# Kernel optimization log

Hardware: AMD Instinct MI355X
Metric: run time of the kernel (lower is better)

## Reference

```python
import jax, jax.numpy as jnp
import numpy as np

DIM = 512   # model dim C (num_heads=1 -> head_dim = C)
NK = 128    # tokens per key-batch element
BQ = 512    # query batch
BK = 256    # key batch
NC = 1000   # num_classes for visual_fc head


def _ln(x, g, b, eps=1e-5):
    m = x.mean(-1, keepdims=True)
    v = x.var(-1, keepdims=True)
    return (x - m) * jax.lax.rsqrt(v + eps) * g + b


def _l2norm(x, eps=1e-12):  # F.normalize(p=2, dim=-1)
    n = jnp.linalg.norm(x, axis=-1, keepdims=True)
    return x / jnp.maximum(n, eps)


def setup_inputs() -> dict:
    key = jax.random.key(0)
    ks = jax.random.split(key, 8)
    s = 0.02
    return {
        "qx": jax.random.normal(ks[0], (BQ, 1, DIM), dtype=jnp.float32),
        "kx": jax.random.normal(ks[1], (BK, NK, DIM), dtype=jnp.float32),
        "key_padding_mask": jax.random.randint(ks[2], (BK, NK), 0, 2).astype(bool),
        "logit_scale": jnp.array([np.log(100.0)], dtype=jnp.float32),
        "g_q": jnp.ones((DIM,), jnp.float32), "b_q": jnp.zeros((DIM,), jnp.float32),
        "g_k": jnp.ones((DIM,), jnp.float32), "b_k": jnp.zeros((DIM,), jnp.float32),
        "wq": jax.random.normal(ks[3], (DIM, DIM), dtype=jnp.float32) * s,
        "wk": jax.random.normal(ks[4], (DIM, DIM), dtype=jnp.float32) * s,
        "w1": jax.random.normal(ks[5], (4 * DIM, DIM), dtype=jnp.float32) * s,
        "b1": jnp.zeros((4 * DIM,), jnp.float32),
        "w2": jax.random.normal(ks[6], (NC, 4 * DIM), dtype=jnp.float32) * s,
        "b2": jnp.zeros((NC,), jnp.float32),
    }


def reference(qx, kx, key_padding_mask, logit_scale,
              g_q, b_q, g_k, b_k, wq, wk, w1, b1, w2, b2):
    C = qx.shape[-1]
    scale = C ** -0.5  # num_heads=1 so head_dim == C
    # cross-batch single-query attention (Attention.forward)
    q = _ln(qx, g_q, b_q) @ wq.T                       # [Bq,1,C]
    k = _ln(kx, g_k, b_k) @ wk.T                       # [Bk,Nk,C]
    attn = jnp.einsum('qoc,knc->qkn', q, k) * scale    # [Bq,Bk,Nk]
    attn = jnp.where(key_padding_mask[None, :, :], -jnp.inf, attn)
    attn = jax.nn.softmax(attn, axis=-1)
    v = jnp.einsum('knc,qkn->qkc', kx, attn)           # [Bq,Bk,C]
    # two_branch head
    h = jax.nn.relu(qx[:, 0, :] @ w1.T + b1)           # [Bq,4C]
    x1 = h @ w2.T + b2                                 # [Bq,NC]
    x2 = jnp.einsum('qkc,qoc->qk', _l2norm(v), _l2norm(qx)) * jnp.exp(logit_scale)[0]
    return (x1, x2)
```

## Files before the change

### kernel.cpp

```cpp
#include <hip/hip_runtime.h>

typedef unsigned short u16;
typedef unsigned int u32;
typedef short bf16x8s __attribute__((ext_vector_type(8)));
typedef float f32x4 __attribute__((ext_vector_type(4)));

#define SCALE_C 0.044194173824159216f
#define MFMA16 __builtin_amdgcn_mfma_f32_16x16x32_bf16

__device__ __forceinline__ u16 f2bf(float f){
  union { float f; u32 u; } c; c.f = f;
  u32 u = c.u;
  return (u16)((u + 0x7fffu + ((u >> 16) & 1u)) >> 16);
}

__device__ __forceinline__ void gload16(const void* g, void* l){
  __builtin_amdgcn_global_load_lds((const __attribute__((address_space(1))) void*)g,
                                   (__attribute__((address_space(3))) void*)l, 16, 0, 0);
}

#define OFF_KXB  ((size_t)0)
#define OFF_G    (OFF_KXB + 33554432)
#define OFF_W2B  (OFF_G + 8388608)
#define OFF_H    (OFF_W2B + 4096000)
#define OFF_W1B  (OFF_H + 2097152)
#define OFF_QLN  (OFF_W1B + 2097152)
#define OFF_QHAT (OFF_QLN + 524288)
#define OFF_QXB  (OFF_QHAT + 524288)
#define OFF_P    (OFF_QXB + 524288)
#define OFF_M2   (OFF_P + 524288)
#define OFF_WQB  (OFF_M2 + 524288)
#define OFF_WCT  (OFF_WQB + 524288)
#define OFF_KM   (OFF_WCT + 524288)
#define OFF_KR   (OFF_KM + 131072)
#define OFF_T2   (OFF_KR + 131072)
#define OFF_FLAG (OFF_T2 + 4096)

__global__ __launch_bounds__(512) void k_phase1(
    const float* __restrict__ qx, const float* __restrict__ kx,
    const int* __restrict__ maskw,
    const float* __restrict__ g_q, const float* __restrict__ b_q,
    const float* __restrict__ wq, const float* __restrict__ wk,
    const float* __restrict__ w1, const float* __restrict__ w2,
    const float* __restrict__ b2,
    u16* __restrict__ kxb, float* __restrict__ km, float* __restrict__ kr,
    u16* __restrict__ Gm,
    u16* __restrict__ qln, u16* __restrict__ qhat, u16* __restrict__ qxb,
    u16* __restrict__ wct, u16* __restrict__ w1b, u16* __restrict__ w2b,
    float* __restrict__ t2s, int* __restrict__ flag, float* __restrict__ x1o)
{
  __shared__ __align__(16) u16 lBig[16384];
  __shared__ float redq[8][2];
  __shared__ int smax;
  const int bid = blockIdx.x, tid = threadIdx.x;
  const int lane = tid & 63, w = tid >> 6;
  const int l15 = lane & 15, lg = lane >> 4;

  if (bid < 256){
    u16* lk = lBig;
    const int z = bid;
    const int a0 = (w>>2)*64, b0 = (w&3)*32;
    float s[16] = {0,0,0,0,0,0,0,0,0,0,0,0,0,0,0,0};
    float sq[16] = {0,0,0,0,0,0,0,0,0,0,0,0,0,0,0,0};
    f32x4 acc[4][2] = {};
    for (int ch = 0; ch < 4; ch++){
      #pragma unroll
      for (int i = 0; i < 16; i++){
        int r = w*16 + i;
        float2 v = *(const float2*)(kx + ((size_t)z*128 + r)*512 + ch*128 + lane*2);
        s[i] += v.x + v.y; sq[i] += v.x*v.x + v.y*v.y;
        u32 pk = f2bf(v.x) | ((u32)f2bf(v.y)<<16);
        *(u32*)(kxb + ((size_t)z*128 + r)*512 + ch*128 + lane*2) = pk;
        *(u32*)&lk[r*128 + ((lane*2) ^ ((r&7)<<3))] = pk;
      }
      __syncthreads();
      #pragma unroll
      for (int kk = 0; kk < 4; kk++){
        int cgr = kk*4 + lg;
        bf16x8s a[4], b[2];
        #pragma unroll
        for (int i2 = 0; i2 < 4; i2++){
          int r = a0 + i2*16 + l15;
          a[i2] = *(const bf16x8s*)&lk[r*128 + ((cgr*8) ^ ((r&7)<<3))];
        }
        #pragma unroll
        for (int j = 0; j < 2; j++){
          int r = b0 + j*16 + l15;
          b[j] = *(const bf16x8s*)&lk[r*128 + ((cgr*8) ^ ((r&7)<<3))];
        }
        #pragma unroll
        for (int i2 = 0; i2 < 4; i2++)
          #pragma unroll
          for (int j = 0; j < 2; j++)
            acc[i2][j] = MFMA16(a[i2], b[j], acc[i2][j], 0,0,0);
      }
      __syncthreads();
    }
    #pragma unroll
    for (int i = 0; i < 16; i++){
      float ss = s[i], qq = sq[i];
      #pragma unroll
      for (int o = 1; o < 64; o <<= 1){ ss += __shfl_xor(ss,o); qq += __shfl_xor(qq,o); }
      if (lane == 0){
        int r = w*16 + i;
        float mean = ss*(1.0f/512.0f);
        float var  = qq*(1.0f/512.0f) - mean*mean;
        km[z*128+r] = mean; kr[z*128+r] = rsqrtf(var + 1e-5f);
      }
    }
    u16* G = Gm + (size_t)z*16384;
    #pragma unroll
    for (int i2 = 0; i2 < 4; i2++)
      #pragma unroll
      for (int j = 0; j < 2; j++)
        #pragma unroll
        for (int r = 0; r < 4; r++)
          G[(size_t)(a0 + i2*16 + lg*4 + r)*128 + b0 + j*16 + l15] = f2bf(acc[i2][j][r]);
  } else if (bid < 512){
    const int row = (bid-256)*2 + (tid>>8);
    const int t = tid & 255;
    float2 v = *(const float2*)(qx + (size_t)row*512 + t*2);
    float s = v.x+v.y, sq = v.x*v.x+v.y*v.y;
    #pragma unroll
    for (int o = 1; o < 64; o <<= 1){ s += __shfl_xor(s,o); sq += __shfl_xor(sq,o); }
    if (lane == 0){ redq[w][0]=s; redq[w][1]=sq; }
    __syncthreads();
    const int h4 = (tid>>8)*4;
    s  = redq[h4][0]+redq[h4+1][0]+redq[h4+2][0]+redq[h4+3][0];
    sq = redq[h4][1]+redq[h4+1][1]+redq[h4+2][1]+redq[h4+3][1];
    float mean = s*(1.0f/512.0f);
    float var  = sq*(1.0f/512.0f) - mean*mean;
    float rstd = rsqrtf(var + 1e-5f);
    float il2  = 1.0f / fmaxf(sqrtf(sq), 1e-12f);
    float2 g  = *(const float2*)(g_q + t*2);
    float2 bb = *(const float2*)(b_q + t*2);
    u32 a  = f2bf((v.x-mean)*rstd*g.x+bb.x) | ((u32)f2bf((v.y-mean)*rstd*g.y+bb.y)<<16);
    u32 hh = f2bf(v.x*il2) | ((u32)f2bf(v.y*il2)<<16);
    u32 xx = f2bf(v.x)     | ((u32)f2bf(v.y)<<16);
    *(u32*)(qln  + (size_t)row*512 + t*2) = a;
    *(u32*)(qhat + (size_t)row*512 + t*2) = hh;
    *(u32*)(qxb  + (size_t)row*512 + t*2) = xx;
  } else if (bid < 2024){
    const float* in; u16* out; int i;
    if (bid < 1024) { in = w1; out = w1b; i = (bid-512)*512 + tid; }
    else            { in = w2; out = w2b; i = (bid-1024)*512 + tid; }
    float4 v = *(const float4*)(in + (size_t)i*4);
    uint2 p;
    p.x = f2bf(v.x)|((u32)f2bf(v.y)<<16); p.y = f2bf(v.z)|((u32)f2bf(v.w)<<16);
    *(uint2*)(out + (size_t)i*4) = p;
  } else if (bid < 2088){
    const int t = bid - 2024;
    const int f0 = (t>>3)*64, c0 = (t&7)*64;
    const int w4 = w & 3;
    const int wr = (w4>>1)*32, wc = (w4&1)*32;
    u16* shA = lBig;
    u16* shB = lBig + 4096;
    f32x4 acc[2][2] = {};
    for (int i0 = 0; i0 < 512; i0 += 64){
      const int ii = tid >> 3;
      const int cc8 = (tid & 7) * 8;
      float4 va0 = *(const float4*)(wk + (size_t)(i0+ii)*512 + f0 + cc8);
      float4 va1 = *(const float4*)(wk + (size_t)(i0+ii)*512 + f0 + cc8 + 4);
      float4 vb0 = *(const float4*)(wq + (size_t)(i0+ii)*512 + c0 + cc8);
      float4 vb1 = *(const float4*)(wq + (size_t)(i0+ii)*512 + c0 + cc8 + 4);
      #pragma unroll
      for (int e = 0; e < 8; e++){
        float fa = e < 4 ? (&va0.x)[e] : (&va1.x)[e-4];
        float fb = e < 4 ? (&vb0.x)[e] : (&vb1.x)[e-4];
        int rowc = cc8 + e;
        int idx = rowc*64 + (((ii>>3) ^ (rowc&7))*8 + (ii&7));
        shA[idx] = f2bf(fa);
        shB[idx] = f2bf(fb);
      }
      __syncthreads();
      #pragma unroll
      for (int kk = 0; kk < 2; kk++){
        int cgr = kk*4 + lg;
        int ra0 = wr + l15, ra1 = wr + 16 + l15;
        int rb0 = wc + l15, rb1 = wc + 16 + l15;
        bf16x8s a0 = *(const bf16x8s*)&shA[ra0*64 + ((cgr ^ (ra0&7))*8)];
        bf16x8s a1 = *(const bf16x8s*)&shA[ra1*64 + ((cgr ^ (ra1&7))*8)];
        bf16x8s b0 = *(const bf16x8s*)&shB[rb0*64 + ((cgr ^ (rb0&7))*8)];
        bf16x8s b1 = *(const bf16x8s*)&shB[rb1*64 + ((cgr ^ (rb1&7))*8)];
        acc[0][0]=MFMA16(a0,b0,acc[0][0],0,0,0);
        acc[0][1]=MFMA16(a0,b1,acc[0][1],0,0,0);
        acc[1][0]=MFMA16(a1,b0,acc[1][0],0,0,0);
        acc[1][1]=MFMA16(a1,b1,acc[1][1],0,0,0);
      }
      __syncthreads();
    }
    if (tid < 256){
      #pragma unroll
      for (int i = 0; i < 2; i++)
        #pragma unroll
        for (int j = 0; j < 2; j++)
          #pragma unroll
          for (int r = 0; r < 4; r++)
            wct[(size_t)(f0 + wr + i*16 + lg*4 + r)*512 + c0 + wc + j*16 + l15]
                = f2bf(acc[i][j][r]);
    }
  } else if (bid < 2338){
    int i = (bid-2088)*2048 + tid*4;
    #pragma unroll
    for (int e = 0; e < 4; e++){
      int idx = i + e;
      x1o[idx] = b2[idx % 1000];
    }
  } else {
    if (tid == 0) smax = 0;
    t2s[tid] = 0.0f;
    __syncthreads();
    int mx = 0;
    for (int i = tid; i < 8192; i += 512){ int v = maskw[i]; mx = v > mx ? v : mx; }
    #pragma unroll
    for (int o = 1; o < 64; o <<= 1){ int t2 = __shfl_xor(mx,o); mx = t2 > mx ? t2 : mx; }
    if ((tid & 63) == 0) atomicMax(&smax, mx);
    __syncthreads();
    if (tid == 0) *flag = (smax <= 1) ? 1 : 0;
  }
}

__device__ __forceinline__ void gemm_body(const u16* __restrict__ Ap, const u16* __restrict__ Bp,
    int M, int N, int K, int m0, int n0, int tid,
    u16 (*lA)[64], u16 (*lB)[64], f32x4 (&acc)[2][2])
{
  const int lane = tid & 63, w = tid >> 6;
  const int wr = (w >> 1)*32, wc = (w & 1)*32;
  const int l15 = lane & 15, lg = lane >> 4;
  for (int kc = 0; kc < K; kc += 64){
    #pragma unroll
    for (int s = 0; s < 2; s++){
      int u = tid + s*256;
      int row = u >> 3, cg = u & 7;
      int sw = (cg ^ (row & 7)) * 8;
      uint4 va = make_uint4(0,0,0,0);
      if (m0 + row < M) va = *(const uint4*)(Ap + (size_t)(m0+row)*K + kc + cg*8);
      *(uint4*)&lA[row][sw] = va;
      uint4 vb = make_uint4(0,0,0,0);
      if (n0 + row < N) vb = *(const uint4*)(Bp + (size_t)(n0+row)*K + kc + cg*8);
      *(uint4*)&lB[row][sw] = vb;
    }
    __syncthreads();
    #pragma unroll
    for (int kk = 0; kk < 2; kk++){
      int cgr = kk*4 + lg;
      int ra0 = wr + l15, ra1 = wr + 16 + l15;
      int rb0 = wc + l15, rb1 = wc + 16 + l15;
      bf16x8s a0 = *(const bf16x8s*)&lA[ra0][(cgr ^ (ra0&7))*8];
      bf16x8s a1 = *(const bf16x8s*)&lA[ra1][(cgr ^ (ra1&7))*8];
      bf16x8s b0 = *(const bf16x8s*)&lB[rb0][(cgr ^ (rb0&7))*8];
      bf16x8s b1 = *(const bf16x8s*)&lB[rb1][(cgr ^ (rb1&7))*8];
      acc[0][0] = MFMA16(a0,b0,acc[0][0],0,0,0);
      acc[0][1] = MFMA16(a0,b1,acc[0][1],0,0,0);
      acc[1][0] = MFMA16(a1,b0,acc[1][0],0,0,0);
      acc[1][1] = MFMA16(a1,b1,acc[1][1],0,0,0);
    }
    __syncthreads();
  }
}

__device__ __forceinline__ void store_tile(void* C, int ldc, int m0, int n0, int M, int N,
    const float* bias, int relu, int bf16out, f32x4 (&acc)[2][2], int tid)
{
  const int lane = tid & 63, w = tid >> 6;
  const int wr = (w >> 1)*32, wc = (w & 1)*32;
  const int l15 = lane & 15, lg = lane >> 4;
  #pragma unroll
  for (int i = 0; i < 2; i++){
    #pragma unroll
    for (int j = 0; j < 2; j++){
      int col = n0 + wc + j*16 + l15;
      if (col < N){
        float bv = bias ? bias[col] : 0.0f;
        #pragma unroll
        for (int r = 0; r < 4; r++){
          int row = m0 + wr + i*16 + lg*4 + r;
          if (row < M){
            float v = acc[i][j][r] + bv;
            if (relu) v = fmaxf(v, 0.0f);
            if (bf16out) ((u16*)C)[(size_t)row*ldc + col] = f2bf(v);
            else         ((float*)C)[(size_t)row*ldc + col] = v;
          }
        }
      }
    }
  }
}

__global__ __launch_bounds__(256) void k_phaseB(
    const u16* __restrict__ qln, const u16* __restrict__ wct,
    const float* __restrict__ g_k, u16* __restrict__ m2, float* __restrict__ t2s,
    const u16* __restrict__ qxb, const u16* __restrict__ w1b,
    const float* __restrict__ b1, u16* __restrict__ hbuf)
{
  __shared__ __align__(16) u16 lA[64][64], lB[64][64];
  f32x4 acc[2][2] = {};
  const int bid = blockIdx.x, tid = threadIdx.x;
  const int lane = tid & 63, w = tid >> 6;
  const int wr = (w >> 1)*32, wc = (w & 1)*32;
  const int l15 = lane & 15, lg = lane >> 4;
  if (bid < 64){
    int m0 = (bid>>3)*64, n0 = (bid&7)*64;
    gemm_body(qln, wct, 512,512,512, m0,n0, tid, lA, lB, acc);
    #pragma unroll
    for (int i = 0; i < 2; i++){
      #pragma unroll
      for (int r = 0; r < 4; r++){
        int row = m0 + wr + i*16 + lg*4 + r;
        float part = 0.f;
        #pragma unroll
        for (int j = 0; j < 2; j++){
          int col = n0 + wc + j*16 + l15;
          float e = SCALE_C * acc[i][j][r] * g_k[col];
          m2[(size_t)row*512 + col] = f2bf(e);
          part += e;
        }
        #pragma unroll
        for (int o = 1; o < 16; o <<= 1) part += __shfl_xor(part, o);
        if (l15 == 0) atomicAdd(&t2s[row], part);
      }
    }
  } else {
    int b = bid-64, m0 = (b>>5)*64, n0 = (b&31)*64;
    gemm_body(qxb, w1b, 512,2048,512, m0,n0, tid, lA, lB, acc);
    store_tile(hbuf, 2048, m0,n0, 512,2048, b1, 1, 1, acc, tid);
  }
}

__global__ __launch_bounds__(256) void k_x1(
    const u16* __restrict__ hbuf, const u16* __restrict__ w2b,
    float* __restrict__ x1o)
{
  __shared__ __align__(16) u16 lA[64][64], lB[64][64];
  const int b = blockIdx.x;
  const int ks = b >> 7;
  const int t  = b & 127;
  const int m0 = (t >> 4)*64, n0 = (t & 15)*64;
  const int tid = threadIdx.x, lane = tid & 63, w = tid >> 6;
  const int wr = (w>>1)*32, wc = (w&1)*32;
  const int l15 = lane & 15, lg = lane >> 4;
  f32x4 acc[2][2] = {};
  for (int kc = ks*512; kc < ks*512 + 512; kc += 64){
    #pragma unroll
    for (int s = 0; s < 2; s++){
      int u = tid + s*256;
      int row = u >> 3, cg = u & 7;
      int sw = (cg ^ (row & 7)) * 8;
      *(uint4*)&lA[row][sw] = *(const uint4*)(hbuf + (size_t)(m0+row)*2048 + kc + cg*8);
      uint4 vb = make_uint4(0,0,0,0);
      if (n0 + row < 1000) vb = *(const uint4*)(w2b + (size_t)(n0+row)*2048 + kc + cg*8);
      *(uint4*)&lB[row][sw] = vb;
    }
    __syncthreads();
    #pragma unroll
    for (int kk = 0; kk < 2; kk++){
      int cgr = kk*4 + lg;
      int ra0 = wr + l15, ra1 = wr + 16 + l15;
      int rb0 = wc + l15, rb1 = wc + 16 + l15;
      bf16x8s a0 = *(const bf16x8s*)&lA[ra0][(cgr ^ (ra0&7))*8];
      bf16x8s a1 = *(const bf16x8s*)&lA[ra1][(cgr ^ (ra1&7))*8];
      bf16x8s b0 = *(const bf16x8s*)&lB[rb0][(cgr ^ (rb0&7))*8];
      bf16x8s b1 = *(const bf16x8s*)&lB[rb1][(cgr ^ (rb1&7))*8];
      acc[0][0]=MFMA16(a0,b0,acc[0][0],0,0,0);
      acc[0][1]=MFMA16(a0,b1,acc[0][1],0,0,0);
      acc[1][0]=MFMA16(a1,b0,acc[1][0],0,0,0);
      acc[1][1]=MFMA16(a1,b1,acc[1][1],0,0,0);
    }
    __syncthreads();
  }
  #pragma unroll
  for (int i = 0; i < 2; i++){
    #pragma unroll
    for (int j = 0; j < 2; j++){
      int col = n0 + wc + j*16 + l15;
      if (col < 1000){
        #pragma unroll
        for (int r = 0; r < 4; r++){
          int row = m0 + wr + i*16 + lg*4 + r;
          atomicAdd(&x1o[(size_t)row*1000 + col], acc[i][j][r]);
        }
      }
    }
  }
}

__global__ __launch_bounds__(512, 4) void k_attn(
    const u16* __restrict__ kxb, const u16* __restrict__ Gm,
    const u16* __restrict__ m2, const u16* __restrict__ qhat,
    const float* __restrict__ km, const float* __restrict__ kr,
    const float* __restrict__ t2s, const void* __restrict__ maskp,
    const int* __restrict__ flagp, const float* __restrict__ lsp,
    float* __restrict__ x2)
{
  __shared__ __align__(16) u16 sb[24576];
  __shared__ float lt2[128];
  __shared__ float lNum[128][2], lDen[128][2];
  u16* lP = sb;

  const int kb = blockIdx.x, q0 = blockIdx.y * 128;
  const int tid = threadIdx.x, lane = tid & 63, w = tid >> 6;
  const int wr = (w >> 1)*32, wcol = (w & 1)*64;
  const int l15 = lane & 15, lg = lane >> 4;
  const int fl = *flagp;
  const float expls = __expf(lsp[0]);

  if (tid < 128) lt2[tid] = t2s[q0 + tid];

  float kmv[4], krv[4], mbv[4];
  #pragma unroll
  for (int j = 0; j < 4; j++){
    int gn = kb*128 + wcol + j*16 + l15;
    kmv[j] = km[gn]; krv[j] = kr[gn];
    int mv = fl ? ((const int*)maskp)[gn] : (int)((const unsigned char*)maskp)[gn];
    mbv[j] = mv ? -1e30f : 0.0f;
  }

  const u16* KX = kxb + (size_t)kb * 65536;
  f32x4 aS[2][4] = {}, aD[2][4] = {};

  const int srow  = w*16 + (lane >> 2);
  const int sslot = (lane & 3) ^ (srow & 3);
  const int lofs  = (w*16)*32;

  #define STAGE(p) do{                                                         \
    const int kc_ = (p)*32;                                                    \
    u16* b_ = sb + ((p)&1)*12288;                                              \
    gload16(KX   + (size_t)srow*512      + kc_ + sslot*8, b_ + lofs);          \
    gload16(m2   + (size_t)(q0+srow)*512 + kc_ + sslot*8, b_ + 4096 + lofs);   \
    gload16(qhat + (size_t)(q0+srow)*512 + kc_ + sslot*8, b_ + 8192 + lofs);   \
  }while(0)

  STAGE(0);
  #pragma unroll
  for (int p = 0; p < 16; p++){
    if (p < 15){
      STAGE(p+1);
      asm volatile("s_waitcnt vmcnt(3)" ::: "memory");
    } else {
      asm volatile("s_waitcnt vmcnt(0)" ::: "memory");
    }
    __builtin_amdgcn_s_barrier();
    __builtin_amdgcn_sched_barrier(0);
    const u16* lb  = sb + (p&1)*12288;
    const u16* lKX = lb;
    const u16* lM2 = lb + 4096;
    const u16* lQH = lb + 8192;
    const int rA0 = wr + l15, rA1 = wr + 16 + l15;
    bf16x8s am0 = *(const bf16x8s*)&lM2[rA0*32 + ((lg ^ (rA0&3))*8)];
    bf16x8s am1 = *(const bf16x8s*)&lM2[rA1*32 + ((lg ^ (rA1&3))*8)];
    bf16x8s aq0 = *(const bf16x8s*)&lQH[rA0*32 + ((lg ^ (rA0&3))*8)];
    bf16x8s aq1 = *(const bf16x8s*)&lQH[rA1*32 + ((lg ^ (rA1&3))*8)];
    __builtin_amdgcn_s_setprio(1);
    #pragma unroll
    for (int j = 0; j < 4; j++){
      int rB = wcol + j*16 + l15;
      bf16x8s bk = *(const bf16x8s*)&lKX[rB*32 + ((lg ^ (rB&3))*8)];
      aS[0][j] = MFMA16(am0, bk, aS[0][j], 0,0,0);
      aS[1][j] = MFMA16(am1, bk, aS[1][j], 0,0,0);
      aD[0][j] = MFMA16(aq0, bk, aD[0][j], 0,0,0);
      aD[1][j] = MFMA16(aq1, bk, aD[1][j], 0,0,0);
    }
    __builtin_amdgcn_s_setprio(0);
    __builtin_amdgcn_sched_barrier(0);
    __builtin_amdgcn_s_barrier();
  }
  __syncthreads();

  #pragma unroll
  for (int i = 0; i < 2; i++){
    #pragma unroll
    for (int r = 0; r < 4; r++){
      int rowl = wr + i*16 + lg*4 + r;
      float t2v = lt2[rowl];
      float sn = 0.f;
      #pragma unroll
      for (int j = 0; j < 4; j++){
        float L = krv[j]*(aS[i][j][r] - kmv[j]*t2v) + mbv[j];
        float e = __expf(L);
        aS[i][j][r] = e;
        sn += e * aD[i][j][r];
      }
      #pragma unroll
      for (int o = 1; o < 16; o <<= 1) sn += __shfl_xor(sn, o);
      if (l15 == 0) lNum[rowl][w&1] = sn;
      #pragma unroll
      for (int j = 0; j < 4; j++){
        int n = wcol + j*16 + l15;
        lP[rowl*128 + ((n>>3)^(rowl&7))*8 + (n&7)] = f2bf(aS[i][j][r]);
      }
    }
  }
  __syncthreads();

  f32x4 aT[2][4] = {};
  const u16* Gk = Gm + (size_t)kb * 16384;
  #pragma unroll
  for (int kk = 0; kk < 4; kk++){
    int cgr = kk*4 + lg;
    int rA0 = wr + l15, rA1 = wr + 16 + l15;
    bf16x8s p0 = *(const bf16x8s*)&lP[rA0*128 + ((cgr^(rA0&7))*8)];
    bf16x8s p1 = *(const bf16x8s*)&lP[rA1*128 + ((cgr^(rA1&7))*8)];
    #pragma unroll
    for (int j = 0; j < 4; j++){
      int mcol = wcol + j*16 + l15;
      bf16x8s bg = *(const bf16x8s*)(Gk + (size_t)mcol*128 + kk*32 + lg*8);
      aT[0][j] = MFMA16(p0, bg, aT[0][j], 0,0,0);
      aT[1][j] = MFMA16(p1, bg, aT[1][j], 0,0,0);
    }
  }
  #pragma unroll
  for (int i = 0; i < 2; i++){
    #pragma unroll
    for (int r = 0; r < 4; r++){
      int rowl = wr + i*16 + lg*4 + r;
      float sd = 0.f;
      #pragma unroll
      for (int j = 0; j < 4; j++) sd += aT[i][j][r] * aS[i][j][r];
      #pragma unroll
      for (int o = 1; o < 16; o <<= 1) sd += __shfl_xor(sd, o);
      if (l15 == 0) lDen[rowl][w&1] = sd;
    }
  }
  __syncthreads();

  if (tid < 128){
    float num  = lNum[tid][0] + lNum[tid][1];
    float den2 = lDen[tid][0] + lDen[tid][1];
    float den  = fmaxf(sqrtf(fmaxf(den2, 0.0f)), 1e-12f);
    x2[(size_t)(q0 + tid)*256 + kb] = expls * num / den;
  }
}

extern "C" void kernel_launch(void* const* d_in, const int* in_sizes, int n_in,
                              void* d_out, int out_size, void* d_ws, size_t ws_size,
                              hipStream_t stream)
{
  (void)in_sizes; (void)n_in; (void)out_size; (void)ws_size;
  const float* qx  = (const float*)d_in[0];
  const float* kx  = (const float*)d_in[1];
  const void*  mask= d_in[2];
  const float* lsp = (const float*)d_in[3];
  const float* g_q = (const float*)d_in[4];
  const float* b_q = (const float*)d_in[5];
  const float* g_k = (const float*)d_in[6];
  const float* wq  = (const float*)d_in[8];
  const float* wk  = (const float*)d_in[9];
  const float* w1  = (const float*)d_in[10];
  const float* b1  = (const float*)d_in[11];
  const float* w2  = (const float*)d_in[12];
  const float* b2  = (const float*)d_in[13];

  char* ws = (char*)d_ws;
  u16* kxb  = (u16*)(ws + OFF_KXB);
  u16* Gm   = (u16*)(ws + OFF_G);
  u16* w2b  = (u16*)(ws + OFF_W2B);
  u16* hbuf = (u16*)(ws + OFF_H);
  u16* w1b  = (u16*)(ws + OFF_W1B);
  u16* qln  = (u16*)(ws + OFF_QLN);
  u16* qhat = (u16*)(ws + OFF_QHAT);
  u16* qxb  = (u16*)(ws + OFF_QXB);
  u16* m2   = (u16*)(ws + OFF_M2);
  u16* wct  = (u16*)(ws + OFF_WCT);
  float* km  = (float*)(ws + OFF_KM);
  float* kr  = (float*)(ws + OFF_KR);
  float* t2s = (float*)(ws + OFF_T2);
  int*   flag= (int*)(ws + OFF_FLAG);
  float* x1o = (float*)d_out;
  float* x2o = (float*)d_out + 512*1000;

  k_phase1<<<dim3(2339), dim3(512), 0, stream>>>(
      qx, kx, (const int*)mask, g_q, b_q, wq, wk, w1, w2, b2,
      kxb, km, kr, Gm, qln, qhat, qxb, wct, w1b, w2b, t2s, flag, x1o);
  k_phaseB<<<dim3(320), dim3(256), 0, stream>>>(
      qln, wct, g_k, m2, t2s, qxb, w1b, b1, hbuf);
  k_x1<<<dim3(512), dim3(256), 0, stream>>>(hbuf, w2b, x1o);
  k_attn<<<dim3(256, 4), dim3(512), 0, stream>>>(
      kxb, Gm, m2, qhat, km, kr, t2s, mask, flag, lsp, x2o);
}
```

Baseline: 132.6 us.

## Fuse first head GEMM into phase1 and merge x1 GEMM into phase2

The qx@w1^T GEMM with bias and ReLU now runs inside phase1, converting fp32 qx and w1 to bf16 on the fly. This removes the separate w1/qx bf16 conversion passes and their buffers. The split-K x1 GEMM moves into the same launch as the wct GEMM, cutting one kernel launch and letting the two run concurrently. The attention kernel's LDS swizzle also changes to XOR with (row>>1)&3, meant to reduce bank conflicts. In exchange, phase1 blocks convert w1 redundantly for each m-tile, and the fused blocks are heavier.

```diff
diff --git a/kernel.cpp b/kernel.cpp
--- a/kernel.cpp
+++ b/kernel.cpp
@@ -41,12 +41,12 @@
     const int* __restrict__ maskw,
     const float* __restrict__ g_q, const float* __restrict__ b_q,
     const float* __restrict__ wq, const float* __restrict__ wk,
-    const float* __restrict__ w1, const float* __restrict__ w2,
-    const float* __restrict__ b2,
+    const float* __restrict__ w1, const float* __restrict__ b1,
+    const float* __restrict__ w2, const float* __restrict__ b2,
     u16* __restrict__ kxb, float* __restrict__ km, float* __restrict__ kr,
     u16* __restrict__ Gm,
-    u16* __restrict__ qln, u16* __restrict__ qhat, u16* __restrict__ qxb,
-    u16* __restrict__ wct, u16* __restrict__ w1b, u16* __restrict__ w2b,
+    u16* __restrict__ qln, u16* __restrict__ qhat,
+    u16* __restrict__ wct, u16* __restrict__ w2b, u16* __restrict__ hbuf,
     float* __restrict__ t2s, int* __restrict__ flag, float* __restrict__ x1o)
 {
   __shared__ __align__(16) u16 lBig[16384];
@@ -136,20 +136,73 @@
     float2 bb = *(const float2*)(b_q + t*2);
     u32 a  = f2bf((v.x-mean)*rstd*g.x+bb.x) | ((u32)f2bf((v.y-mean)*rstd*g.y+bb.y)<<16);
     u32 hh = f2bf(v.x*il2) | ((u32)f2bf(v.y*il2)<<16);
-    u32 xx = f2bf(v.x)     | ((u32)f2bf(v.y)<<16);
     *(u32*)(qln  + (size_t)row*512 + t*2) = a;
     *(u32*)(qhat + (size_t)row*512 + t*2) = hh;
-    *(u32*)(qxb  + (size_t)row*512 + t*2) = xx;
-  } else if (bid < 2024){
-    const float* in; u16* out; int i;
-    if (bid < 1024) { in = w1; out = w1b; i = (bid-512)*512 + tid; }
-    else            { in = w2; out = w2b; i = (bid-1024)*512 + tid; }
-    float4 v = *(const float4*)(in + (size_t)i*4);
+  } else if (bid < 1512){
+    int i = (bid-512)*512 + tid;
+    float4 v = *(const float4*)(w2 + (size_t)i*4);
     uint2 p;
     p.x = f2bf(v.x)|((u32)f2bf(v.y)<<16); p.y = f2bf(v.z)|((u32)f2bf(v.w)<<16);
-    *(uint2*)(out + (size_t)i*4) = p;
-  } else if (bid < 2088){
-    const int t = bid - 2024;
+    *(uint2*)(w2b + (size_t)i*4) = p;
+  } else if (bid < 1640){
+    const int t = bid - 1512;
+    const int m0 = (t >> 4)*64, n0 = (t & 15)*128;
+    const int w4 = w & 3;
+    const int nb = (w >> 2)*64;
+    const int wr = (w4>>1)*32, wc = (w4&1)*32;
+    u16* shA = lBig;
+    u16* shB = lBig + 4096;
+    f32x4 acc[2][2] = {};
+    for (int kc = 0; kc < 512; kc += 64){
+      {
+        int row = tid >> 3, c8 = (tid & 7)*8;
+        float4 a0 = *(const float4*)(qx + (size_t)(m0+row)*512 + kc + c8);
+        float4 a1 = *(const float4*)(qx + (size_t)(m0+row)*512 + kc + c8 + 4);
+        u16 ta[8] = {f2bf(a0.x),f2bf(a0.y),f2bf(a0.z),f2bf(a0.w),
+                     f2bf(a1.x),f2bf(a1.y),f2bf(a1.z),f2bf(a1.w)};
+        *(uint4*)&shA[row*64 + (((tid&7) ^ (row&7))*8)] = *(uint4*)ta;
+        #pragma unroll
+        for (int s2 = 0; s2 < 2; s2++){
+          int u = tid + s2*512;
+          int rowb = u >> 3, cb8 = (u & 7)*8;
+          float4 b0 = *(const float4*)(w1 + (size_t)(n0+rowb)*512 + kc + cb8);
+          float4 b1v = *(const float4*)(w1 + (size_t)(n0+rowb)*512 + kc + cb8 + 4);
+          u16 tb[8] = {f2bf(b0.x),f2bf(b0.y),f2bf(b0.z),f2bf(b0.w),
+                       f2bf(b1v.x),f2bf(b1v.y),f2bf(b1v.z),f2bf(b1v.w)};
+          *(uint4*)&shB[rowb*64 + (((u&7) ^ (rowb&7))*8)] = *(uint4*)tb;
+        }
+      }
+      __syncthreads();
+      #pragma unroll
+      for (int kk = 0; kk < 2; kk++){
+        int cgr = kk*4 + lg;
+        int ra0 = wr + l15, ra1 = wr + 16 + l15;
+        int rb0 = nb + wc + l15, rb1 = nb + wc + 16 + l15;
+        bf16x8s a0 = *(const bf16x8s*)&shA[ra0*64 + ((cgr ^ (ra0&7))*8)];
+        bf16x8s a1 = *(const bf16x8s*)&shA[ra1*64 + ((cgr ^ (ra1&7))*8)];
+        bf16x8s b0 = *(const bf16x8s*)&shB[rb0*64 + ((cgr ^ (rb0&7))*8)];
+        bf16x8s b1 = *(const bf16x8s*)&shB[rb1*64 + ((cgr ^ (rb1&7))*8)];
+        acc[0][0]=MFMA16(a0,b0,acc[0][0],0,0,0);
+        acc[0][1]=MFMA16(a0,b1,acc[0][1],0,0,0);
+        acc[1][0]=MFMA16(a1,b0,acc[1][0],0,0,0);
+        acc[1][1]=MFMA16(a1,b1,acc[1][1],0,0,0);
+      }
+      __syncthreads();
+    }
+    #pragma unroll
+    for (int i = 0; i < 2; i++)
+      #pragma unroll
+      for (int j = 0; j < 2; j++){
+        int col = n0 + nb + wc + j*16 + l15;
+        float bv = b1[col];
+        #pragma unroll
+        for (int r = 0; r < 4; r++){
+          int row = m0 + wr + i*16 + lg*4 + r;
+          hbuf[(size_t)row*2048 + col] = f2bf(fmaxf(acc[i][j][r] + bv, 0.0f));
+        }
+      }
+  } else if (bid < 1704){
+    const int t = bid - 1640;
     const int f0 = (t>>3)*64, c0 = (t&7)*64;
     const int w4 = w & 3;
     const int wr = (w4>>1)*32, wc = (w4&1)*32;
@@ -199,8 +252,8 @@
             wct[(size_t)(f0 + wr + i*16 + lg*4 + r)*512 + c0 + wc + j*16 + l15]
                 = f2bf(acc[i][j][r]);
     }
-  } else if (bid < 2338){
-    int i = (bid-2088)*2048 + tid*4;
+  } else if (bid < 1954){
+    int i = (bid-1704)*2048 + tid*4;
     #pragma unroll
     for (int e = 0; e < 4; e++){
       int idx = i + e;
@@ -259,39 +312,11 @@
   }
 }
 
-__device__ __forceinline__ void store_tile(void* C, int ldc, int m0, int n0, int M, int N,
-    const float* bias, int relu, int bf16out, f32x4 (&acc)[2][2], int tid)
-{
-  const int lane = tid & 63, w = tid >> 6;
-  const int wr = (w >> 1)*32, wc = (w & 1)*32;
-  const int l15 = lane & 15, lg = lane >> 4;
-  #pragma unroll
-  for (int i = 0; i < 2; i++){
-    #pragma unroll
-    for (int j = 0; j < 2; j++){
-      int col = n0 + wc + j*16 + l15;
-      if (col < N){
-        float bv = bias ? bias[col] : 0.0f;
-        #pragma unroll
-        for (int r = 0; r < 4; r++){
-          int row = m0 + wr + i*16 + lg*4 + r;
-          if (row < M){
-            float v = acc[i][j][r] + bv;
-            if (relu) v = fmaxf(v, 0.0f);
-            if (bf16out) ((u16*)C)[(size_t)row*ldc + col] = f2bf(v);
-            else         ((float*)C)[(size_t)row*ldc + col] = v;
-          }
-        }
-      }
-    }
-  }
-}
-
-__global__ __launch_bounds__(256) void k_phaseB(
+__global__ __launch_bounds__(256) void k_phase2(
     const u16* __restrict__ qln, const u16* __restrict__ wct,
     const float* __restrict__ g_k, u16* __restrict__ m2, float* __restrict__ t2s,
-    const u16* __restrict__ qxb, const u16* __restrict__ w1b,
-    const float* __restrict__ b1, u16* __restrict__ hbuf)
+    const u16* __restrict__ hbuf, const u16* __restrict__ w2b,
+    float* __restrict__ x1o)
 {
   __shared__ __align__(16) u16 lA[64][64], lB[64][64];
   f32x4 acc[2][2] = {};
@@ -299,8 +324,54 @@
   const int lane = tid & 63, w = tid >> 6;
   const int wr = (w >> 1)*32, wc = (w & 1)*32;
   const int l15 = lane & 15, lg = lane >> 4;
-  if (bid < 64){
-    int m0 = (bid>>3)*64, n0 = (bid&7)*64;
+  if (bid < 512){
+    const int ks = bid >> 7;
+    const int t  = bid & 127;
+    const int m0 = (t >> 4)*64, n0 = (t & 15)*64;
+    for (int kc = ks*512; kc < ks*512 + 512; kc += 64){
+      #pragma unroll
+      for (int s = 0; s < 2; s++){
+        int u = tid + s*256;
+        int row = u >> 3, cg = u & 7;
+        int sw = (cg ^ (row & 7)) * 8;
+        *(uint4*)&lA[row][sw] = *(const uint4*)(hbuf + (size_t)(m0+row)*2048 + kc + cg*8);
+        uint4 vb = make_uint4(0,0,0,0);
+        if (n0 + row < 1000) vb = *(const uint4*)(w2b + (size_t)(n0+row)*2048 + kc + cg*8);
+        *(uint4*)&lB[row][sw] = vb;
+      }
+      __syncthreads();
+      #pragma unroll
+      for (int kk = 0; kk < 2; kk++){
+        int cgr = kk*4 + lg;
+        int ra0 = wr + l15, ra1 = wr + 16 + l15;
+        int rb0 = wc + l15, rb1 = wc + 16 + l15;
+        bf16x8s a0 = *(const bf16x8s*)&lA[ra0][(cgr ^ (ra0&7))*8];
+        bf16x8s a1 = *(const bf16x8s*)&lA[ra1][(cgr ^ (ra1&7))*8];
+        bf16x8s b0 = *(const bf16x8s*)&lB[rb0][(cgr ^ (rb0&7))*8];
+        bf16x8s b1 = *(const bf16x8s*)&lB[rb1][(cgr ^ (rb1&7))*8];
+        acc[0][0]=MFMA16(a0,b0,acc[0][0],0,0,0);
+        acc[0][1]=MFMA16(a0,b1,acc[0][1],0,0,0);
+        acc[1][0]=MFMA16(a1,b0,acc[1][0],0,0,0);
+        acc[1][1]=MFMA16(a1,b1,acc[1][1],0,0,0);
+      }
+      __syncthreads();
+    }
+    #pragma unroll
+    for (int i = 0; i < 2; i++)
+      #pragma unroll
+      for (int j = 0; j < 2; j++){
+        int col = n0 + wc + j*16 + l15;
+        if (col < 1000){
+          #pragma unroll
+          for (int r = 0; r < 4; r++){
+            int row = m0 + wr + i*16 + lg*4 + r;
+            atomicAdd(&x1o[(size_t)row*1000 + col], acc[i][j][r]);
+          }
+        }
+      }
+  } else {
+    const int b = bid - 512;
+    int m0 = (b>>3)*64, n0 = (b&7)*64;
     gemm_body(qln, wct, 512,512,512, m0,n0, tid, lA, lB, acc);
     #pragma unroll
     for (int i = 0; i < 2; i++){
@@ -318,67 +389,6 @@
         #pragma unroll
         for (int o = 1; o < 16; o <<= 1) part += __shfl_xor(part, o);
         if (l15 == 0) atomicAdd(&t2s[row], part);
-      }
-    }
-  } else {
-    int b = bid-64, m0 = (b>>5)*64, n0 = (b&31)*64;
-    gemm_body(qxb, w1b, 512,2048,512, m0,n0, tid, lA, lB, acc);
-    store_tile(hbuf, 2048, m0,n0, 512,2048, b1, 1, 1, acc, tid);
-  }
-}
-
-__global__ __launch_bounds__(256) void k_x1(
-    const u16* __restrict__ hbuf, const u16* __restrict__ w2b,
-    float* __restrict__ x1o)
-{
-  __shared__ __align__(16) u16 lA[64][64], lB[64][64];
-  const int b = blockIdx.x;
-  const int ks = b >> 7;
-  const int t  = b & 127;
-  const int m0 = (t >> 4)*64, n0 = (t & 15)*64;
-  const int tid = threadIdx.x, lane = tid & 63, w = tid >> 6;
-  const int wr = (w>>1)*32, wc = (w&1)*32;
-  const int l15 = lane & 15, lg = lane >> 4;
-  f32x4 acc[2][2] = {};
-  for (int kc = ks*512; kc < ks*512 + 512; kc += 64){
-    #pragma unroll
-    for (int s = 0; s < 2; s++){
-      int u = tid + s*256;
-      int row = u >> 3, cg = u & 7;
-      int sw = (cg ^ (row & 7)) * 8;
-      *(uint4*)&lA[row][sw] = *(const uint4*)(hbuf + (size_t)(m0+row)*2048 + kc + cg*8);
-      uint4 vb = make_uint4(0,0,0,0);
-      if (n0 + row < 1000) vb = *(const uint4*)(w2b + (size_t)(n0+row)*2048 + kc + cg*8);
-      *(uint4*)&lB[row][sw] = vb;
-    }
-    __syncthreads();
-    #pragma unroll
-    for (int kk = 0; kk < 2; kk++){
-      int cgr = kk*4 + lg;
-      int ra0 = wr + l15, ra1 = wr + 16 + l15;
-      int rb0 = wc + l15, rb1 = wc + 16 + l15;
-      bf16x8s a0 = *(const bf16x8s*)&lA[ra0][(cgr ^ (ra0&7))*8];
-      bf16x8s a1 = *(const bf16x8s*)&lA[ra1][(cgr ^ (ra1&7))*8];
-      bf16x8s b0 = *(const bf16x8s*)&lB[rb0][(cgr ^ (rb0&7))*8];
-      bf16x8s b1 = *(const bf16x8s*)&lB[rb1][(cgr ^ (rb1&7))*8];
-      acc[0][0]=MFMA16(a0,b0,acc[0][0],0,0,0);
-      acc[0][1]=MFMA16(a0,b1,acc[0][1],0,0,0);
-      acc[1][0]=MFMA16(a1,b0,acc[1][0],0,0,0);
-      acc[1][1]=MFMA16(a1,b1,acc[1][1],0,0,0);
-    }
-    __syncthreads();
-  }
-  #pragma unroll
-  for (int i = 0; i < 2; i++){
-    #pragma unroll
-    for (int j = 0; j < 2; j++){
-      int col = n0 + wc + j*16 + l15;
-      if (col < 1000){
-        #pragma unroll
-        for (int r = 0; r < 4; r++){
-          int row = m0 + wr + i*16 + lg*4 + r;
-          atomicAdd(&x1o[(size_t)row*1000 + col], acc[i][j][r]);
-        }
       }
     }
   }
@@ -419,8 +429,8 @@
   f32x4 aS[2][4] = {}, aD[2][4] = {};
 
   const int srow  = w*16 + (lane >> 2);
-  const int sslot = (lane & 3) ^ (srow & 3);
-  const int lofs  = (w*16)*32;
+  const int sslot = (lane & 3) ^ ((srow >> 1) & 3);
+  const int lofs  = w*512;
 
   #define STAGE(p) do{                                                         \
     const int kc_ = (p)*32;                                                    \
@@ -446,15 +456,15 @@
     const u16* lM2 = lb + 4096;
     const u16* lQH = lb + 8192;
     const int rA0 = wr + l15, rA1 = wr + 16 + l15;
-    bf16x8s am0 = *(const bf16x8s*)&lM2[rA0*32 + ((lg ^ (rA0&3))*8)];
-    bf16x8s am1 = *(const bf16x8s*)&lM2[rA1*32 + ((lg ^ (rA1&3))*8)];
-    bf16x8s aq0 = *(const bf16x8s*)&lQH[rA0*32 + ((lg ^ (rA0&3))*8)];
-    bf16x8s aq1 = *(const bf16x8s*)&lQH[rA1*32 + ((lg ^ (rA1&3))*8)];
+    bf16x8s am0 = *(const bf16x8s*)&lM2[rA0*32 + ((lg ^ ((rA0>>1)&3))*8)];
+    bf16x8s am1 = *(const bf16x8s*)&lM2[rA1*32 + ((lg ^ ((rA1>>1)&3))*8)];
+    bf16x8s aq0 = *(const bf16x8s*)&lQH[rA0*32 + ((lg ^ ((rA0>>1)&3))*8)];
+    bf16x8s aq1 = *(const bf16x8s*)&lQH[rA1*32 + ((lg ^ ((rA1>>1)&3))*8)];
     __builtin_amdgcn_s_setprio(1);
     #pragma unroll
     for (int j = 0; j < 4; j++){
       int rB = wcol + j*16 + l15;
-      bf16x8s bk = *(const bf16x8s*)&lKX[rB*32 + ((lg ^ (rB&3))*8)];
+      bf16x8s bk = *(const bf16x8s*)&lKX[rB*32 + ((lg ^ ((rB>>1)&3))*8)];
       aS[0][j] = MFMA16(am0, bk, aS[0][j], 0,0,0);
       aS[1][j] = MFMA16(am1, bk, aS[1][j], 0,0,0);
       aD[0][j] = MFMA16(aq0, bk, aD[0][j], 0,0,0);
@@ -555,10 +565,8 @@
   u16* Gm   = (u16*)(ws + OFF_G);
   u16* w2b  = (u16*)(ws + OFF_W2B);
   u16* hbuf = (u16*)(ws + OFF_H);
-  u16* w1b  = (u16*)(ws + OFF_W1B);
   u16* qln  = (u16*)(ws + OFF_QLN);
   u16* qhat = (u16*)(ws + OFF_QHAT);
-  u16* qxb  = (u16*)(ws + OFF_QXB);
   u16* m2   = (u16*)(ws + OFF_M2);
   u16* wct  = (u16*)(ws + OFF_WCT);
   float* km  = (float*)(ws + OFF_KM);
@@ -568,12 +576,11 @@
   float* x1o = (float*)d_out;
   float* x2o = (float*)d_out + 512*1000;
 
-  k_phase1<<<dim3(2339), dim3(512), 0, stream>>>(
-      qx, kx, (const int*)mask, g_q, b_q, wq, wk, w1, w2, b2,
-      kxb, km, kr, Gm, qln, qhat, qxb, wct, w1b, w2b, t2s, flag, x1o);
-  k_phaseB<<<dim3(320), dim3(256), 0, stream>>>(
-      qln, wct, g_k, m2, t2s, qxb, w1b, b1, hbuf);
-  k_x1<<<dim3(512), dim3(256), 0, stream>>>(hbuf, w2b, x1o);
+  k_phase1<<<dim3(1955), dim3(512), 0, stream>>>(
+      qx, kx, (const int*)mask, g_q, b_q, wq, wk, w1, b1, w2, b2,
+      kxb, km, kr, Gm, qln, qhat, wct, w2b, hbuf, t2s, flag, x1o);
+  k_phase2<<<dim3(576), dim3(256), 0, stream>>>(
+      qln, wct, g_k, m2, t2s, hbuf, w2b, x1o);
   k_attn<<<dim3(256, 4), dim3(512), 0, stream>>>(
       kxb, Gm, m2, qhat, km, kr, t2s, mask, flag, lsp, x2o);
 }
```

New measurement: 121.3 us. -8.5%, faster.
